# Kernel optimization log

Hardware: AMD Instinct MI355X
Metric: run time of the kernel (lower is better)

The kernel has to match this reference:

```python
import jax, jax.numpy as jnp
import numpy as np

THETA = 40.0  # Gaussian edge temperature from __init__(theta=40)


def _unfold3(x):
    """torch F.unfold(kernel=3, pad=1, stride=1) reshaped to (n, c, 9, h, w).
    Kernel positions are enumerated row-major (ki*3 + kj), matching torch."""
    n, c, h, w = x.shape
    xp = jnp.pad(x, ((0, 0), (0, 0), (1, 1), (1, 1)))
    return jnp.stack(
        [xp[:, :, ki:ki + h, kj:kj + w] for ki in range(3) for kj in range(3)],
        axis=2,
    )


def setup_inputs() -> dict:
    key = jax.random.key(0)
    k1, k2 = jax.random.split(key)
    mask = jax.random.normal(k1, (8, 19, 256, 256), dtype=jnp.float32)
    edge = jax.random.uniform(k2, (8, 1, 256, 256), dtype=jnp.float32)
    return {"mask": mask, "edge": edge, "iter_n": 2}


def reference(mask, edge, iter_n):
    max_edge = edge.max()
    # local_edge: (n, 1, 9, h, w) = center edge + 3x3 neighborhood edge
    local_edge = edge[:, :, None, :, :] + _unfold3(edge)
    # softmax over the 9 neighborhood positions (max_edge shift is a
    # softmax-invariant stabilizer, kept for faithfulness)
    weights = jax.nn.softmax(-THETA * (local_edge - max_edge), axis=2)
    # iterative edge-guided 3x3 weighted-sum stencil on the mask
    for _ in range(iter_n):
        mask = (_unfold3(mask) * weights).sum(axis=2)
    return mask
```

## Files before the change

kernel.cpp:

```cpp
#include <hip/hip_runtime.h>


#define HH 256
#define WW 256
#define NC 19
#define THETA 40.0f

__global__ __launch_bounds__(1024)
void geg_fused_kernel(const float* __restrict__ mask,
                      const float* __restrict__ edge,
                      float* __restrict__ out) {
    const int tid = threadIdx.x;
    const int ox = blockIdx.x * 32;
    const int oy = blockIdx.y * 32;
    const int n  = blockIdx.z;

    __shared__ float e_lds[36][37];
    __shared__ float m_lds[36][37];
    __shared__ float t_lds[34][36];

    const float* eptr = edge + (size_t)n * HH * WW;
    for (int i = tid; i < 36 * 36; i += 1024) {
        int y = i / 36, x = i - y * 36;
        int gy = oy + y - 2, gx = ox + x - 2;
        float v = 0.f;
        if ((unsigned)gy < HH && (unsigned)gx < WW) v = eptr[gy * WW + gx];
        e_lds[y][x] = v;
    }
    __syncthreads();

    const int yy1 = (tid >> 5) + 1, xx1 = (tid & 31) + 1;
    const bool has2 = tid < 132;
    int yy2 = 0, xx2 = 0;
    if (has2) {
        if (tid < 34)       { yy2 = 0;          xx2 = tid;       }
        else if (tid < 68)  { yy2 = 33;         xx2 = tid - 34;  }
        else if (tid < 100) { yy2 = tid - 67;   xx2 = 0;         }
        else                { yy2 = tid - 99;   xx2 = 33;        }
    }

    float wA[9], wB[9];
    {
        float lg[9], mx = -1e30f;
        #pragma unroll
        for (int k = 0; k < 9; ++k) {
            int ki = k / 3, kj = k - ki * 3;
            lg[k] = -THETA * e_lds[yy1 + ki][xx1 + kj];
            mx = fmaxf(mx, lg[k]);
        }
        float s = 0.f;
        #pragma unroll
        for (int k = 0; k < 9; ++k) { wA[k] = __expf(lg[k] - mx); s += wA[k]; }
        float inv = 1.f / s;
        #pragma unroll
        for (int k = 0; k < 9; ++k) wA[k] *= inv;
    }
    if (has2) {
        float lg[9], mx = -1e30f;
        #pragma unroll
        for (int k = 0; k < 9; ++k) {
            int ki = k / 3, kj = k - ki * 3;
            lg[k] = -THETA * e_lds[yy2 + ki][xx2 + kj];
            mx = fmaxf(mx, lg[k]);
        }
        float s = 0.f;
        #pragma unroll
        for (int k = 0; k < 9; ++k) { wB[k] = __expf(lg[k] - mx); s += wB[k]; }
        float inv = 1.f / s;
        #pragma unroll
        for (int k = 0; k < 9; ++k) wB[k] *= inv;
    }
    const int g2y = oy + yy2 - 1, g2x = ox + xx2 - 1;
    const bool v2 = has2 && (unsigned)g2y < HH && (unsigned)g2x < WW;

    const size_t img = (size_t)HH * WW;
    const float* mbase = mask + (size_t)n * NC * img;
    float*       obase = out  + (size_t)n * NC * img;
    const int goy = oy + yy1 - 1, gox = ox + xx1 - 1;

    for (int c = 0; c < NC; ++c) {
        const float* mp = mbase + (size_t)c * img;
        __syncthreads();
        for (int i = tid; i < 36 * 36; i += 1024) {
            int y = i / 36, x = i - y * 36;
            int gy = oy + y - 2, gx = ox + x - 2;
            float v = 0.f;
            if ((unsigned)gy < HH && (unsigned)gx < WW) v = mp[gy * WW + gx];
            m_lds[y][x] = v;
        }
        __syncthreads();

        {
            float s = 0.f;
            #pragma unroll
            for (int k = 0; k < 9; ++k) {
                int ki = k / 3, kj = k - ki * 3;
                s += wA[k] * m_lds[yy1 + ki][xx1 + kj];
            }
            t_lds[yy1][xx1] = s;
        }
        if (has2) {
            float s = 0.f;
            #pragma unroll
            for (int k = 0; k < 9; ++k) {
                int ki = k / 3, kj = k - ki * 3;
                s += wB[k] * m_lds[yy2 + ki][xx2 + kj];
            }
            t_lds[yy2][xx2] = v2 ? s : 0.f;
        }
        __syncthreads();

        {
            float s = 0.f;
            #pragma unroll
            for (int k = 0; k < 9; ++k) {
                int ki = k / 3, kj = k - ki * 3;
                s += wA[k] * t_lds[yy1 - 1 + ki][xx1 - 1 + kj];
            }
            obase[(size_t)c * img + (size_t)goy * WW + gox] = s;
        }
    }
}

extern "C" void kernel_launch(void* const* d_in, const int* in_sizes, int n_in,
                              void* d_out, int out_size, void* d_ws, size_t ws_size,
                              hipStream_t stream) {
    const float* mask = (const float*)d_in[0];
    const float* edge = (const float*)d_in[1];
    float* out = (float*)d_out;

    dim3 grid(WW / 32, HH / 32, 8);
    geg_fused_kernel<<<grid, 1024, 0, stream>>>(mask, edge, out);
}
```

Before: 37.16 us.

## Register-prefetch mask channels two ahead and double-buffer LDS to drop a barrier

Mask tiles for upcoming channels are now loaded into registers two iterations ahead, so global-memory latency overlaps with the stencil math of the current channel. The m_lds and t_lds buffers are double-buffered by channel parity, which removes one of the three barriers per channel. Load indices and offsets are computed once outside the loop, and launch bounds request two blocks per CU. The cost is more registers and LDS per block, which could limit occupancy or cause spills given the weight arrays held in registers.

```diff
diff --git a/kernel.cpp b/kernel.cpp
--- a/kernel.cpp
+++ b/kernel.cpp
@@ -6,7 +6,7 @@
 #define NC 19
 #define THETA 40.0f
 
-__global__ __launch_bounds__(1024)
+__global__ __launch_bounds__(1024, 2)
 void geg_fused_kernel(const float* __restrict__ mask,
                       const float* __restrict__ edge,
                       float* __restrict__ out) {
@@ -16,17 +16,36 @@
     const int n  = blockIdx.z;
 
     __shared__ float e_lds[36][37];
-    __shared__ float m_lds[36][37];
-    __shared__ float t_lds[34][36];
+    __shared__ float m_lds[2][36][37];
+    __shared__ float t_lds[2][34][36];
 
-    const float* eptr = edge + (size_t)n * HH * WW;
-    for (int i = tid; i < 36 * 36; i += 1024) {
-        int y = i / 36, x = i - y * 36;
-        int gy = oy + y - 2, gx = ox + x - 2;
-        float v = 0.f;
-        if ((unsigned)gy < HH && (unsigned)gx < WW) v = eptr[gy * WW + gx];
-        e_lds[y][x] = v;
-    }
+    const size_t img = (size_t)HH * WW;
+    const float* mbase = mask + (size_t)n * NC * img;
+    const float* eptr  = edge + (size_t)n * img;
+
+    const int y0 = tid / 36, x0 = tid - y0 * 36;
+    const int i1 = tid + 1024;
+    const int y1 = i1 / 36, x1 = i1 - y1 * 36;
+    const bool s1v = (i1 < 36 * 36);
+    const int gy0 = oy + y0 - 2, gx0 = ox + x0 - 2;
+    const int gy1 = oy + y1 - 2, gx1 = ox + x1 - 2;
+    const bool in0 = (unsigned)gy0 < HH && (unsigned)gx0 < WW;
+    const bool in1 = s1v && (unsigned)gy1 < HH && (unsigned)gx1 < WW;
+    const int off0 = in0 ? (gy0 * WW + gx0) : 0;
+    const int off1 = in1 ? (gy1 * WW + gx1) : 0;
+
+    e_lds[y0][x0] = in0 ? eptr[off0] : 0.f;
+    if (s1v) e_lds[y1][x1] = in1 ? eptr[off1] : 0.f;
+
+    const float* q0 = mbase + off0;
+    const float* q1 = mbase + off1;
+    float cur0 = in0 ? q0[0]   : 0.f;
+    float cur1 = in1 ? q1[0]   : 0.f;
+    float nxt0 = in0 ? q0[img] : 0.f;
+    float nxt1 = in1 ? q1[img] : 0.f;
+    const float* pf0 = q0 + 2 * img;
+    const float* pf1 = q1 + 2 * img;
+
     __syncthreads();
 
     const int yy1 = (tid >> 5) + 1, xx1 = (tid & 31) + 1;
@@ -73,20 +92,40 @@
     const int g2y = oy + yy2 - 1, g2x = ox + xx2 - 1;
     const bool v2 = has2 && (unsigned)g2y < HH && (unsigned)g2x < WW;
 
-    const size_t img = (size_t)HH * WW;
-    const float* mbase = mask + (size_t)n * NC * img;
-    float*       obase = out  + (size_t)n * NC * img;
-    const int goy = oy + yy1 - 1, gox = ox + xx1 - 1;
+    float* op = out + (size_t)n * NC * img
+                    + (size_t)(oy + yy1 - 1) * WW + (ox + xx1 - 1);
 
     for (int c = 0; c < NC; ++c) {
-        const float* mp = mbase + (size_t)c * img;
+        const int b = c & 1;
+
+        m_lds[b][y0][x0] = cur0;
+        if (s1v) m_lds[b][y1][x1] = cur1;
         __syncthreads();
-        for (int i = tid; i < 36 * 36; i += 1024) {
-            int y = i / 36, x = i - y * 36;
-            int gy = oy + y - 2, gx = ox + x - 2;
-            float v = 0.f;
-            if ((unsigned)gy < HH && (unsigned)gx < WW) v = mp[gy * WW + gx];
-            m_lds[y][x] = v;
+
+        float fu0 = 0.f, fu1 = 0.f;
+        if (c + 2 < NC) {
+            fu0 = in0 ? pf0[0] : 0.f;
+            fu1 = in1 ? pf1[0] : 0.f;
+            pf0 += img; pf1 += img;
+        }
+
+        {
+            float s = 0.f;
+            #pragma unroll
+            for (int k = 0; k < 9; ++k) {
+                int ki = k / 3, kj = k - ki * 3;
+                s += wA[k] * m_lds[b][yy1 + ki][xx1 + kj];
+            }
+            t_lds[b][yy1][xx1] = s;
+        }
+        if (has2) {
+            float s = 0.f;
+            #pragma unroll
+            for (int k = 0; k < 9; ++k) {
+                int ki = k / 3, kj = k - ki * 3;
+                s += wB[k] * m_lds[b][yy2 + ki][xx2 + kj];
+            }
+            t_lds[b][yy2][xx2] = v2 ? s : 0.f;
         }
         __syncthreads();
 
@@ -95,30 +134,14 @@
             #pragma unroll
             for (int k = 0; k < 9; ++k) {
                 int ki = k / 3, kj = k - ki * 3;
-                s += wA[k] * m_lds[yy1 + ki][xx1 + kj];
+                s += wA[k] * t_lds[b][yy1 - 1 + ki][xx1 - 1 + kj];
             }
-            t_lds[yy1][xx1] = s;
+            *op = s;
+            op += img;
         }
-        if (has2) {
-            float s = 0.f;
-            #pragma unroll
-            for (int k = 0; k < 9; ++k) {
-                int ki = k / 3, kj = k - ki * 3;
-                s += wB[k] * m_lds[yy2 + ki][xx2 + kj];
-            }
-            t_lds[yy2][xx2] = v2 ? s : 0.f;
-        }
-        __syncthreads();
 
-        {
-            float s = 0.f;
-            #pragma unroll
-            for (int k = 0; k < 9; ++k) {
-                int ki = k / 3, kj = k - ki * 3;
-                s += wA[k] * t_lds[yy1 - 1 + ki][xx1 - 1 + kj];
-            }
-            obase[(size_t)c * img + (size_t)goy * WW + gox] = s;
-        }
+        cur0 = nxt0; cur1 = nxt1;
+        nxt0 = fu0;  nxt1 = fu1;
     }
 }
 
```

After: 29.90 us. -19.5%, faster.
